# Optimization experiments

Hardware: AMD Instinct MI355X
Metric: run time of the kernel (lower is better)

## Reference

```python
import jax, jax.numpy as jnp
import numpy as np

N = 50000          # nodes
E = 800000         # edges (avg in-degree 16)
NFEAT, F = 128, 64 # input feat, hidden width (outfeat = outd_1 = outd_2 = 64)
ALPHA = 0.2        # leaky relu slope
AVG_LIN = 16.0             # sum(bin*hist)/N for deg histogram (all deg 16)
AVG_LOG = float(np.log(17.0))  # sum(log(bin+1)*hist)/N


def setup_inputs():
    key = jax.random.key(0)
    ks = jax.random.split(key, 16)
    g = lambda i, shp, s: (jax.random.normal(ks[i], shp, jnp.float32) * s)
    return {
        "x": g(0, (N, NFEAT), 1.0),
        "adj": jnp.zeros((1,), jnp.float32),
        "edge_index": jax.random.randint(ks[1], (2, E), 0, N, dtype=jnp.int32),
        "W0": g(2, (NFEAT, F), NFEAT ** -0.5), "b0": jnp.zeros((F,), jnp.float32),
        "c1_pre_W": g(3, (2 * F, F), (2 * F) ** -0.5), "c1_pre_b": jnp.zeros((F,), jnp.float32),
        "c1_post_W": g(4, (5 * F, F), (5 * F) ** -0.5), "c1_post_b": jnp.zeros((F,), jnp.float32),
        "c1_lin_W": g(5, (F, F), F ** -0.5), "c1_lin_b": jnp.zeros((F,), jnp.float32),
        "c2_pre_W": g(6, (2 * F, F), (2 * F) ** -0.5), "c2_pre_b": jnp.zeros((F,), jnp.float32),
        "c2_post_W": g(7, (5 * F, F), (5 * F) ** -0.5), "c2_post_b": jnp.zeros((F,), jnp.float32),
        "c2_lin_W": g(8, (F, F), F ** -0.5), "c2_lin_b": jnp.zeros((F,), jnp.float32),
        "W2": g(9, (F, 1), F ** -0.5), "b2": jnp.zeros((1,), jnp.float32),
    }


def pna_conv(x, src, dst, pre_W, pre_b, post_W, post_b, lin_W, lin_b):
    # message: pre_nn(cat[x_i, x_j]) per edge  (x_i = target, x_j = source)
    h = jnp.concatenate([x[dst], x[src]], axis=-1) @ pre_W + pre_b  # [E, F]
    cnt = jax.ops.segment_sum(jnp.ones((h.shape[0],), h.dtype), dst, num_segments=N)
    deg = jnp.clip(cnt, 1.0)                                        # [N]
    mean = jax.ops.segment_sum(h, dst, num_segments=N) / deg[:, None]
    mx = jax.ops.segment_max(h, dst, num_segments=N)
    mx = jnp.where(cnt[:, None] > 0, mx, 0.0)                       # empty segs -> 0
    agg = jnp.concatenate([mean, mx], axis=-1)                      # [N, 2F]
    att = agg * (AVG_LOG / jnp.log(deg + 1.0))[:, None]             # attenuation scaler
    lin = agg * (deg / AVG_LIN)[:, None]                            # linear scaler
    out = jnp.concatenate([x, att, lin], axis=-1)                   # [N, 5F]
    out = out @ post_W + post_b
    return out @ lin_W + lin_b


def reference(x, adj, edge_index, W0, b0,
              c1_pre_W, c1_pre_b, c1_post_W, c1_post_b, c1_lin_W, c1_lin_b,
              c2_pre_W, c2_pre_b, c2_post_W, c2_post_b, c2_lin_W, c2_lin_b,
              W2, b2):
    src, dst = edge_index[0], edge_index[1]
    h = jax.nn.leaky_relu(x @ W0 + b0, negative_slope=ALPHA)  # dropout = id (eval)
    h = jax.nn.relu(pna_conv(h, src, dst, c1_pre_W, c1_pre_b, c1_post_W, c1_post_b, c1_lin_W, c1_lin_b))
    h = jax.nn.relu(pna_conv(h, src, dst, c2_pre_W, c2_pre_b, c2_post_W, c2_post_b, c2_lin_W, c2_lin_b))
    return h @ W2 + b2  # [N, 1]
```

## Files before the change

kernel.cpp:

```cpp
#include <hip/hip_runtime.h>
#include <hip/hip_bf16.h>

typedef __hip_bfloat16 bf16;
typedef unsigned short u16;
typedef unsigned int u32;
typedef __attribute__((ext_vector_type(8))) short short8;
typedef __attribute__((ext_vector_type(4))) float f32x4;

static constexpr float AVG_LOG_C = 2.8332133440562162f;
#define BCAP 1024
#define CHUNK 4096
#define PREP_TOTAL (8192 * 3 + 20480 * 2 + 64 * 6 + 1)

__device__ __forceinline__ u32 f2bf_bits(float f) {
    u32 u = __float_as_uint(f);
    return (u + 0x7fffu + ((u >> 16) & 1u)) >> 16;
}
__device__ __forceinline__ float bf2f(u16 b) {
    return __uint_as_float(((u32)b) << 16);
}

__global__ __launch_bounds__(1024) void detect_zero_kernel(
    const u32* __restrict__ xwords, int* __restrict__ flag,
    int* __restrict__ bcnt, int nb) {
    if (blockIdx.x == 0) {
        int tid = threadIdx.x;
        if (tid < 64) {
            int good = 0;
            for (int i = tid; i < 2048; i += 64) {
                u32 lo = xwords[i] & 0xffffu;
                float v = __uint_as_float(lo << 16);
                float a = fabsf(v);
                if (v == 0.0f || (a >= 1e-3f && a <= 100.0f)) good++;
            }
            for (int off = 32; off; off >>= 1) good += __shfl_xor(good, off, 64);
            if (tid == 0) *flag = (2 * good > 2048) ? 1 : 0;
        }
    } else {
        int i = (blockIdx.x - 1) * 1024 + threadIdx.x;
        if (i < nb) bcnt[i] = 0;
    }
}

__global__ __launch_bounds__(1024) void prep_scatter_kernel(
    const int* __restrict__ srcs, const int* __restrict__ dsts,
    int* __restrict__ bcnt, u32* __restrict__ bstage, int e, int nb,
    const void* __restrict__ W0r,  const void* __restrict__ b0r,
    const void* __restrict__ pre1r, const void* __restrict__ preb1r,
    const void* __restrict__ post1r, const void* __restrict__ postb1r,
    const void* __restrict__ lin1r, const void* __restrict__ linb1r,
    const void* __restrict__ pre2r, const void* __restrict__ preb2r,
    const void* __restrict__ post2r, const void* __restrict__ postb2r,
    const void* __restrict__ lin2r, const void* __restrict__ linb2r,
    const void* __restrict__ W2r,  const void* __restrict__ b2r,
    u16* __restrict__ W0p, u16* __restrict__ pre1p, u16* __restrict__ pre2p,
    u16* __restrict__ wf1p, u16* __restrict__ wf2p,
    float* __restrict__ bfo1, float* __restrict__ bfo2,
    float* __restrict__ preb1f, float* __restrict__ preb2f,
    float* __restrict__ b0f, float* __restrict__ W2f, float* __restrict__ b2f,
    const int* __restrict__ flag) {
    __shared__ int lhist[2048];
    __shared__ int lbase[2048];
    int tid = threadIdx.x;
    int scatB = (e + CHUNK - 1) / CHUNK;
    if ((int)blockIdx.x < scatB) {
        int cbase = blockIdx.x * CHUNK;
        for (int b = tid; b < nb; b += 1024) lhist[b] = 0;
        __syncthreads();
#pragma unroll
        for (int i = 0; i < CHUNK; i += 1024) {
            int e0 = cbase + i + tid;
            if (e0 < e) atomicAdd(&lhist[dsts[e0] >> 5], 1);
        }
        __syncthreads();
        for (int b = tid; b < nb; b += 1024) {
            int c = lhist[b];
            lbase[b] = c ? atomicAdd(&bcnt[b], c) : 0;
            lhist[b] = 0;
        }
        __syncthreads();
#pragma unroll
        for (int i = 0; i < CHUNK; i += 1024) {
            int e0 = cbase + i + tid;
            if (e0 < e) {
                int d = dsts[e0];
                int b = d >> 5;
                int pos = lbase[b] + atomicAdd(&lhist[b], 1);
                if (pos < BCAP)
                    bstage[(size_t)b * BCAP + pos] = (u32)srcs[e0] | ((u32)(d & 31) << 17);
            }
        }
        return;
    }
    int idx = ((int)blockIdx.x - scatB) * 1024 + tid;
    bool isbf = (*flag) != 0;
    auto ld = [&](const void* p, int i) -> float {
        return isbf ? bf2f(((const u16*)p)[i]) : ((const float*)p)[i];
    };
    if (idx < 8192) {
        int j = idx & 7, l = (idx >> 3) & 63, tt = idx >> 9;
        int c = tt & 3, s = tt >> 2;
        int kk = s * 32 + (l >> 4) * 8 + j;
        int col = c * 16 + (l & 15);
        W0p[idx] = (u16)f2bf_bits(ld(W0r, kk * 64 + col));
        return;
    }
    idx -= 8192;
    for (int which = 0; which < 2; ++which) {
        if (idx < 8192) {
            const void* src = which ? pre2r : pre1r;
            u16* dst = which ? pre2p : pre1p;
            int j = idx & 7, l = (idx >> 3) & 63, tt = idx >> 9;
            int c = tt & 7, s = tt >> 3;
            int kk = s * 32 + (l >> 4) * 8 + j;
            int col = c * 16 + (l & 15);
            float v = (col < 64) ? ld(src, kk * 64 + col)
                                 : ld(src, (64 + kk) * 64 + (col - 64));
            dst[idx] = (u16)f2bf_bits(v);
            return;
        }
        idx -= 8192;
    }
    for (int which = 0; which < 2; ++which) {
        if (idx < 20480) {
            const void* postW = which ? post2r : post1r;
            const void* linW  = which ? lin2r  : lin1r;
            u16* dst = which ? wf2p : wf1p;
            int j = idx & 7, l = (idx >> 3) & 63, tt = idx >> 9;
            int c = tt & 3, s = tt >> 2;
            int kk = s * 32 + (l >> 4) * 8 + j;
            int col = c * 16 + (l & 15);
            float a = 0.f;
            for (int k = 0; k < 64; ++k)
                a = fmaf(ld(postW, kk * 64 + k), ld(linW, k * 64 + col), a);
            dst[idx] = (u16)f2bf_bits(a);
            return;
        }
        idx -= 20480;
    }
    for (int which = 0; which < 2; ++which) {
        if (idx < 64) {
            const void* postb = which ? postb2r : postb1r;
            const void* linW  = which ? lin2r : lin1r;
            const void* linb  = which ? linb2r : linb1r;
            float* dst = which ? bfo2 : bfo1;
            float a = ld(linb, idx);
            for (int k = 0; k < 64; ++k)
                a = fmaf(ld(postb, k), ld(linW, k * 64 + idx), a);
            dst[idx] = a;
            return;
        }
        idx -= 64;
    }
    if (idx < 64) { preb1f[idx] = ld(preb1r, idx); return; }
    idx -= 64;
    if (idx < 64) { preb2f[idx] = ld(preb2r, idx); return; }
    idx -= 64;
    if (idx < 64) { b0f[idx] = ld(b0r, idx); return; }
    idx -= 64;
    if (idx < 64) { W2f[idx] = ld(W2r, idx); return; }
    idx -= 64;
    if (idx < 1) { b2f[0] = ld(b2r, 0); }
}

__global__ __launch_bounds__(512, 6) void gemm_x_pq_kernel(
    const void* __restrict__ xraw, const u16* __restrict__ W0p,
    const float* __restrict__ b0f, const u16* __restrict__ pre1p,
    u16* __restrict__ hA, u16* __restrict__ PQ,
    const int* __restrict__ flag, int n) {
    __shared__ __align__(16) u16 xsh[32 * 136];
    __shared__ __align__(16) u16 hsh[32 * 72];
    int tid = threadIdx.x;
    int wave = __builtin_amdgcn_readfirstlane(tid >> 6);
    int lane = tid & 63;
    int blockbase = blockIdx.x * 32;
    bool isbf = (*flag) != 0;
    {
        int row = tid >> 4;
        int cg = (tid & 15) * 8;
        int grow = blockbase + row;
        short8 v = short8{0, 0, 0, 0, 0, 0, 0, 0};
        if (grow < n) {
            if (isbf) {
                v = *(const short8*)((const u16*)xraw + (size_t)grow * 128 + cg);
            } else {
                const float* xf = (const float*)xraw + (size_t)grow * 128 + cg;
                f32x4 a0 = *(const f32x4*)xf;
                f32x4 a1 = *(const f32x4*)(xf + 4);
#pragma unroll
                for (int j = 0; j < 4; ++j) {
                    v[j]     = (short)f2bf_bits(a0[j]);
                    v[4 + j] = (short)f2bf_bits(a1[j]);
                }
            }
        }
        *(short8*)&xsh[row * 136 + cg] = v;
    }
    __syncthreads();
    int rt = wave & 1, ct = wave >> 1;
    int arl = rt * 16 + (lane & 15);
    int koff = (lane >> 4) * 8;
    f32x4 acc = f32x4{0.f, 0.f, 0.f, 0.f};
#pragma unroll
    for (int s = 0; s < 4; ++s) {
        short8 a = *(const short8*)&xsh[arl * 136 + s * 32 + koff];
        short8 b = *(const short8*)(W0p + ((size_t)(s * 4 + ct) * 64 + lane) * 8);
        acc = __builtin_amdgcn_mfma_f32_16x16x32_bf16(a, b, acc, 0, 0, 0);
    }
    {
        int col = ct * 16 + (lane & 15);
        float bv = b0f[col];
        int r0l = rt * 16 + (lane >> 4) * 4;
#pragma unroll
        for (int r = 0; r < 4; ++r) {
            float v = acc[r] + bv;
            v = v > 0.f ? v : 0.2f * v;
            u16 bits = (u16)f2bf_bits(v);
            hsh[(r0l + r) * 72 + col] = bits;
            int grow = blockbase + r0l + r;
            if (grow < n) hA[(size_t)grow * 64 + col] = bits;
        }
    }
    __syncthreads();
#pragma unroll
    for (int half = 0; half < 2; ++half) {
        int tile = wave * 2 + half;
        int rt2 = tile & 1, ct2 = tile >> 1;
        int ar2 = rt2 * 16 + (lane & 15);
        f32x4 acc2 = f32x4{0.f, 0.f, 0.f, 0.f};
#pragma unroll
        for (int s = 0; s < 2; ++s) {
            short8 a = *(const short8*)&hsh[ar2 * 72 + s * 32 + koff];
            short8 b = *(const short8*)(pre1p + ((size_t)(s * 8 + ct2) * 64 + lane) * 8);
            acc2 = __builtin_amdgcn_mfma_f32_16x16x32_bf16(a, b, acc2, 0, 0, 0);
        }
        int col2 = ct2 * 16 + (lane & 15);
        int r02 = rt2 * 16 + (lane >> 4) * 4;
#pragma unroll
        for (int r = 0; r < 4; ++r) {
            int grow = blockbase + r02 + r;
            if (grow < n) PQ[(size_t)grow * 128 + col2] = (u16)f2bf_bits(acc2[r]);
        }
    }
}

template<int FINAL>
__global__ __launch_bounds__(512, 6) void agg_gemm_kernel(
    const u16* __restrict__ PQ, const u16* __restrict__ h,
    const u32* __restrict__ bstage, const int* __restrict__ bcnt,
    const float* __restrict__ prebf, const u16* __restrict__ Wfp,
    const float* __restrict__ bfo, const u16* __restrict__ prenextp,
    u16* __restrict__ hout, u16* __restrict__ PQout,
    const float* __restrict__ W2f, const float* __restrict__ b2f,
    void* __restrict__ out, const int* __restrict__ flag, int n) {
    constexpr int PAD = 328;
    __shared__ __align__(16) u16 vsh[32 * PAD];
    __shared__ __align__(16) u16 hsh[32 * 72];
    __shared__ u32 lel[BCAP];
    __shared__ int loff[32], lcnt[32], lcur[32];
    __shared__ float fsum[32];
    int tid = threadIdx.x;
    int wave = __builtin_amdgcn_readfirstlane(tid >> 6);
    int lane = tid & 63;
    int b = blockIdx.x;
    int blockbase = b * 32;
    float pbl = prebf[lane];
    if (tid < 32) { lcnt[tid] = 0; if (FINAL) fsum[tid] = 0.f; }
    __syncthreads();
    int cb = min(bcnt[b], BCAP);
    const u32* st = bstage + (size_t)b * BCAP;
    for (int i = tid; i < cb; i += 512) atomicAdd(&lcnt[st[i] >> 17], 1);
    __syncthreads();
    if (wave == 0) {
        int c = (lane < 32) ? lcnt[lane] : 0;
        int s = c;
        for (int off = 1; off < 32; off <<= 1) {
            int t = __shfl_up(s, (unsigned)off, 64);
            if (lane >= off) s += t;
        }
        if (lane < 32) {
            loff[lane] = s - c;
            lcur[lane] = s - c;
        }
    }
    __syncthreads();
    for (int i = tid; i < cb; i += 512) {
        u32 e = st[i];
        int pos = atomicAdd(&lcur[e >> 17], 1);
        lel[pos] = (e & 0x1ffffu) << 8;
    }
    __syncthreads();
    const char* PQc = (const char*)PQ;
    u32 voffb = 128u + 2u * (u32)lane;
#pragma unroll
    for (int t = 0; t < 4; ++t) {
        int nl = wave * 4 + t;
        int node = blockbase + nl;
        u16* vrow = &vsh[nl * PAD];
        if (node < n) {
            int beg = loff[nl], end = beg + lcnt[nl];
            int cnt = end - beg;
            float s = 0.f, m = -3.4e38f;
            int e = beg;
            for (; e + 8 <= end; e += 8) {
                float q0 = bf2f(*(const u16*)(PQc + lel[e]     + voffb));
                float q1 = bf2f(*(const u16*)(PQc + lel[e + 1] + voffb));
                float q2 = bf2f(*(const u16*)(PQc + lel[e + 2] + voffb));
                float q3 = bf2f(*(const u16*)(PQc + lel[e + 3] + voffb));
                float q4 = bf2f(*(const u16*)(PQc + lel[e + 4] + voffb));
                float q5 = bf2f(*(const u16*)(PQc + lel[e + 5] + voffb));
                float q6 = bf2f(*(const u16*)(PQc + lel[e + 6] + voffb));
                float q7 = bf2f(*(const u16*)(PQc + lel[e + 7] + voffb));
                s += ((q0 + q1) + (q2 + q3)) + ((q4 + q5) + (q6 + q7));
                m = fmaxf(m, fmaxf(fmaxf(fmaxf(q0, q1), fmaxf(q2, q3)),
                                   fmaxf(fmaxf(q4, q5), fmaxf(q6, q7))));
            }
            for (; e + 4 <= end; e += 4) {
                float q0 = bf2f(*(const u16*)(PQc + lel[e]     + voffb));
                float q1 = bf2f(*(const u16*)(PQc + lel[e + 1] + voffb));
                float q2 = bf2f(*(const u16*)(PQc + lel[e + 2] + voffb));
                float q3 = bf2f(*(const u16*)(PQc + lel[e + 3] + voffb));
                s += (q0 + q1) + (q2 + q3);
                m = fmaxf(fmaxf(m, fmaxf(q0, q1)), fmaxf(q2, q3));
            }
            for (; e < end; ++e) {
                float q = bf2f(*(const u16*)(PQc + lel[e] + voffb));
                s += q;
                m = fmaxf(m, q);
            }
            float mean, mx, deg;
            if (cnt > 0) {
                deg = (float)cnt;
                float p = bf2f(PQ[(size_t)node * 128 + lane]) + pbl;
                mean = p + s / deg;
                mx = p + m;
            } else {
                deg = 1.f; mean = 0.f; mx = 0.f;
            }
            float att = AVG_LOG_C / logf(deg + 1.f);
            float lin = deg * (1.f / 16.f);
            vrow[lane]       = h[(size_t)node * 64 + lane];
            vrow[64 + lane]  = (u16)f2bf_bits(att * mean);
            vrow[128 + lane] = (u16)f2bf_bits(att * mx);
            vrow[192 + lane] = (u16)f2bf_bits(lin * mean);
            vrow[256 + lane] = (u16)f2bf_bits(lin * mx);
        } else {
            vrow[lane] = 0; vrow[64 + lane] = 0; vrow[128 + lane] = 0;
            vrow[192 + lane] = 0; vrow[256 + lane] = 0;
        }
    }
    __syncthreads();
    int rt = wave & 1, ct = wave >> 1;
    int arl = rt * 16 + (lane & 15);
    int koff = (lane >> 4) * 8;
    f32x4 acc = f32x4{0.f, 0.f, 0.f, 0.f};
#pragma unroll
    for (int s = 0; s < 10; ++s) {
        short8 a = *(const short8*)&vsh[arl * PAD + s * 32 + koff];
        short8 b2 = *(const short8*)(Wfp + ((size_t)(s * 4 + ct) * 64 + lane) * 8);
        acc = __builtin_amdgcn_mfma_f32_16x16x32_bf16(a, b2, acc, 0, 0, 0);
    }
    int col = ct * 16 + (lane & 15);
    float bv = bfo[col];
    int r0l = rt * 16 + (lane >> 4) * 4;
    if constexpr (!FINAL) {
#pragma unroll
        for (int r = 0; r < 4; ++r) {
            float v = fmaxf(acc[r] + bv, 0.f);
            u16 bits = (u16)f2bf_bits(v);
            hsh[(r0l + r) * 72 + col] = bits;
            int grow = blockbase + r0l + r;
            if (grow < n) hout[(size_t)grow * 64 + col] = bits;
        }
        __syncthreads();
#pragma unroll
        for (int half = 0; half < 2; ++half) {
            int tile = wave * 2 + half;
            int rt2 = tile & 1, ct2 = tile >> 1;
            int ar2 = rt2 * 16 + (lane & 15);
            f32x4 acc2 = f32x4{0.f, 0.f, 0.f, 0.f};
#pragma unroll
            for (int s = 0; s < 2; ++s) {
                short8 a = *(const short8*)&hsh[ar2 * 72 + s * 32 + koff];
                short8 b2 = *(const short8*)(prenextp + ((size_t)(s * 8 + ct2) * 64 + lane) * 8);
                acc2 = __builtin_amdgcn_mfma_f32_16x16x32_bf16(a, b2, acc2, 0, 0, 0);
            }
            int col2 = ct2 * 16 + (lane & 15);
            int r02 = rt2 * 16 + (lane >> 4) * 4;
#pragma unroll
            for (int r = 0; r < 4; ++r) {
                int grow = blockbase + r02 + r;
                if (grow < n) PQout[(size_t)grow * 128 + col2] = (u16)f2bf_bits(acc2[r]);
            }
        }
    } else {
        float w2 = W2f[col];
        float part[4];
#pragma unroll
        for (int r = 0; r < 4; ++r)
            part[r] = fmaxf(acc[r] + bv, 0.f) * w2;
#pragma unroll
        for (int r = 0; r < 4; ++r) {
            float v = part[r];
            v += __shfl_xor(v, 1, 64);
            v += __shfl_xor(v, 2, 64);
            v += __shfl_xor(v, 4, 64);
            v += __shfl_xor(v, 8, 64);
            if ((lane & 15) == 0) atomicAdd(&fsum[r0l + r], v);
        }
        __syncthreads();
        if (tid < 32) {
            int grow = blockbase + tid;
            if (grow < n) {
                float res = fsum[tid] + b2f[0];
                if (*flag) ((u16*)out)[grow] = (u16)f2bf_bits(res);
                else       ((float*)out)[grow] = res;
            }
        }
    }
}

extern "C" void kernel_launch(void* const* d_in, const int* in_sizes, int n_in,
                              void* d_out, int out_size, void* d_ws, size_t ws_size,
                              hipStream_t stream) {
    const int N = in_sizes[0] / 128;
    const int E = in_sizes[2] / 2;
    const int nb = (N + 31) >> 5;
    const int* ei = (const int*)d_in[2];
    const int* esrc = ei;
    const int* edst = ei + E;

    char* w = (char*)d_ws;
    auto alloc = [&](size_t bytes) -> void* {
        void* p = (void*)w;
        w += (bytes + 255) & ~(size_t)255;
        return p;
    };
    int* flag    = (int*)alloc(4);
    int* bcnt    = (int*)alloc((size_t)nb * 4);
    u32* bstage  = (u32*)alloc((size_t)nb * BCAP * 4);
    u16* W0p     = (u16*)alloc(128 * 64 * 2);
    u16* pre1p   = (u16*)alloc(64 * 128 * 2);
    u16* pre2p   = (u16*)alloc(64 * 128 * 2);
    u16* wf1p    = (u16*)alloc(320 * 64 * 2);
    u16* wf2p    = (u16*)alloc(320 * 64 * 2);
    float* bfo1  = (float*)alloc(64 * 4);
    float* bfo2  = (float*)alloc(64 * 4);
    float* preb1f= (float*)alloc(64 * 4);
    float* preb2f= (float*)alloc(64 * 4);
    float* b0f   = (float*)alloc(64 * 4);
    float* W2f   = (float*)alloc(64 * 4);
    float* b2f_  = (float*)alloc(4);
    u16* hA      = (u16*)alloc((size_t)N * 64 * 2);
    u16* hB      = (u16*)alloc((size_t)N * 64 * 2);
    u16* PQA     = (u16*)alloc((size_t)N * 128 * 2);
    u16* PQB     = (u16*)alloc((size_t)N * 128 * 2);

    detect_zero_kernel<<<1 + (nb + 1023) / 1024, 1024, 0, stream>>>(
        (const u32*)d_in[0], flag, bcnt, nb);

    int scatB = (E + CHUNK - 1) / CHUNK;
    int prepB = (PREP_TOTAL + 1023) / 1024;
    prep_scatter_kernel<<<scatB + prepB, 1024, 0, stream>>>(
        esrc, edst, bcnt, bstage, E, nb,
        d_in[3], d_in[4], d_in[5], d_in[6], d_in[7], d_in[8], d_in[9], d_in[10],
        d_in[11], d_in[12], d_in[13], d_in[14], d_in[15], d_in[16], d_in[17], d_in[18],
        W0p, pre1p, pre2p, wf1p, wf2p,
        bfo1, bfo2, preb1f, preb2f, b0f, W2f, b2f_, flag);

    int gblocks = (N + 31) / 32;
    gemm_x_pq_kernel<<<gblocks, 512, 0, stream>>>(
        d_in[0], W0p, b0f, pre1p, hA, PQA, flag, N);

    agg_gemm_kernel<0><<<gblocks, 512, 0, stream>>>(
        PQA, hA, bstage, bcnt, preb1f, wf1p, bfo1, pre2p, hB, PQB,
        nullptr, nullptr, nullptr, flag, N);

    agg_gemm_kernel<1><<<gblocks, 512, 0, stream>>>(
        PQB, hB, bstage, bcnt, preb2f, wf2p, bfo2, nullptr, nullptr, nullptr,
        W2f, b2f_, d_out, flag, N);
}
```

Baseline: 204.6 us.

## Fuse scatter, first GEMM and both PNA aggregations into cooperative persistent kernel

```diff
diff --git a/kernel.cpp b/kernel.cpp
--- a/kernel.cpp
+++ b/kernel.cpp
@@ -1,5 +1,8 @@
 #include <hip/hip_runtime.h>
 #include <hip/hip_bf16.h>
+#include <hip/hip_cooperative_groups.h>
+
+namespace cg = cooperative_groups;
 
 typedef __hip_bfloat16 bf16;
 typedef unsigned short u16;
@@ -9,7 +12,7 @@
 
 static constexpr float AVG_LOG_C = 2.8332133440562162f;
 #define BCAP 1024
-#define CHUNK 4096
+#define CHUNK 2048
 #define PREP_TOTAL (8192 * 3 + 20480 * 2 + 64 * 6 + 1)
 
 __device__ __forceinline__ u32 f2bf_bits(float f) {
@@ -20,31 +23,31 @@
     return __uint_as_float(((u32)b) << 16);
 }
 
-__global__ __launch_bounds__(1024) void detect_zero_kernel(
+struct KParams {
+    const void* xraw;
+    const int* srcs;
+    const int* dsts;
+    int* bcnt;
+    u32* bstage;
+    const u16 *W0p, *pre1p, *pre2p, *wf1p, *wf2p;
+    const float *b0f, *preb1f, *preb2f, *bfo1, *bfo2, *W2f, *b2f;
+    u16 *hA, *hB, *PQA, *PQB;
+    void* out;
+    const int* flag;
+    int n, e, nb, scatChunks, gB;
+};
+
+struct SMem {
+    union {
+        struct { int lhist[2048]; int lbase[2048]; } sc;
+        struct { __align__(16) u16 xsh[32 * 136]; __align__(16) u16 hsh[32 * 72]; } gx;
+        struct { __align__(16) u16 vsh[32 * 328]; __align__(16) u16 hsh[32 * 72];
+                 u32 lel[BCAP]; int loff[32]; int lcnt[32]; int lcur[32]; float fsum[32]; } ag;
+    };
+};
+
+__global__ __launch_bounds__(1024) void prep_weights_kernel(
     const u32* __restrict__ xwords, int* __restrict__ flag,
-    int* __restrict__ bcnt, int nb) {
-    if (blockIdx.x == 0) {
-        int tid = threadIdx.x;
-        if (tid < 64) {
-            int good = 0;
-            for (int i = tid; i < 2048; i += 64) {
-                u32 lo = xwords[i] & 0xffffu;
-                float v = __uint_as_float(lo << 16);
-                float a = fabsf(v);
-                if (v == 0.0f || (a >= 1e-3f && a <= 100.0f)) good++;
-            }
-            for (int off = 32; off; off >>= 1) good += __shfl_xor(good, off, 64);
-            if (tid == 0) *flag = (2 * good > 2048) ? 1 : 0;
-        }
-    } else {
-        int i = (blockIdx.x - 1) * 1024 + threadIdx.x;
-        if (i < nb) bcnt[i] = 0;
-    }
-}
-
-__global__ __launch_bounds__(1024) void prep_scatter_kernel(
-    const int* __restrict__ srcs, const int* __restrict__ dsts,
-    int* __restrict__ bcnt, u32* __restrict__ bstage, int e, int nb,
     const void* __restrict__ W0r,  const void* __restrict__ b0r,
     const void* __restrict__ pre1r, const void* __restrict__ preb1r,
     const void* __restrict__ post1r, const void* __restrict__ postb1r,
@@ -57,46 +60,27 @@
     u16* __restrict__ wf1p, u16* __restrict__ wf2p,
     float* __restrict__ bfo1, float* __restrict__ bfo2,
     float* __restrict__ preb1f, float* __restrict__ preb2f,
-    float* __restrict__ b0f, float* __restrict__ W2f, float* __restrict__ b2f,
-    const int* __restrict__ flag) {
-    __shared__ int lhist[2048];
-    __shared__ int lbase[2048];
+    float* __restrict__ b0f, float* __restrict__ W2f, float* __restrict__ b2f) {
+    __shared__ int sflag;
     int tid = threadIdx.x;
-    int scatB = (e + CHUNK - 1) / CHUNK;
-    if ((int)blockIdx.x < scatB) {
-        int cbase = blockIdx.x * CHUNK;
-        for (int b = tid; b < nb; b += 1024) lhist[b] = 0;
-        __syncthreads();
-#pragma unroll
-        for (int i = 0; i < CHUNK; i += 1024) {
-            int e0 = cbase + i + tid;
-            if (e0 < e) atomicAdd(&lhist[dsts[e0] >> 5], 1);
-        }
-        __syncthreads();
-        for (int b = tid; b < nb; b += 1024) {
-            int c = lhist[b];
-            lbase[b] = c ? atomicAdd(&bcnt[b], c) : 0;
-            lhist[b] = 0;
-        }
-        __syncthreads();
-#pragma unroll
-        for (int i = 0; i < CHUNK; i += 1024) {
-            int e0 = cbase + i + tid;
-            if (e0 < e) {
-                int d = dsts[e0];
-                int b = d >> 5;
-                int pos = lbase[b] + atomicAdd(&lhist[b], 1);
-                if (pos < BCAP)
-                    bstage[(size_t)b * BCAP + pos] = (u32)srcs[e0] | ((u32)(d & 31) << 17);
-            }
-        }
-        return;
-    }
-    int idx = ((int)blockIdx.x - scatB) * 1024 + tid;
-    bool isbf = (*flag) != 0;
+    if (tid < 64) {
+        int good = 0;
+        for (int i = tid; i < 2048; i += 64) {
+            u32 lo = xwords[i] & 0xffffu;
+            float v = __uint_as_float(lo << 16);
+            float a = fabsf(v);
+            if (v == 0.0f || (a >= 1e-3f && a <= 100.0f)) good++;
+        }
+        for (int off = 32; off; off >>= 1) good += __shfl_xor(good, off, 64);
+        if (tid == 0) sflag = (2 * good > 2048) ? 1 : 0;
+    }
+    __syncthreads();
+    bool isbf = sflag != 0;
+    if (blockIdx.x == 0 && tid == 0) *flag = sflag;
     auto ld = [&](const void* p, int i) -> float {
         return isbf ? bf2f(((const u16*)p)[i]) : ((const float*)p)[i];
     };
+    int idx = (int)blockIdx.x * 1024 + tid;
     if (idx < 8192) {
         int j = idx & 7, l = (idx >> 3) & 63, tt = idx >> 9;
         int c = tt & 3, s = tt >> 2;
@@ -163,28 +147,48 @@
     if (idx < 1) { b2f[0] = ld(b2r, 0); }
 }
 
-__global__ __launch_bounds__(512, 6) void gemm_x_pq_kernel(
-    const void* __restrict__ xraw, const u16* __restrict__ W0p,
-    const float* __restrict__ b0f, const u16* __restrict__ pre1p,
-    u16* __restrict__ hA, u16* __restrict__ PQ,
-    const int* __restrict__ flag, int n) {
-    __shared__ __align__(16) u16 xsh[32 * 136];
-    __shared__ __align__(16) u16 hsh[32 * 72];
-    int tid = threadIdx.x;
-    int wave = __builtin_amdgcn_readfirstlane(tid >> 6);
-    int lane = tid & 63;
-    int blockbase = blockIdx.x * 32;
-    bool isbf = (*flag) != 0;
+__device__ __forceinline__ void scatter_chunk(SMem& sm, const KParams& p, int chunk, int tid) {
+    for (int bb = tid; bb < p.nb; bb += 512) sm.sc.lhist[bb] = 0;
+    __syncthreads();
+    int cbase = chunk * CHUNK;
+#pragma unroll
+    for (int i = 0; i < CHUNK; i += 512) {
+        int e0 = cbase + i + tid;
+        if (e0 < p.e) atomicAdd(&sm.sc.lhist[p.dsts[e0] >> 5], 1);
+    }
+    __syncthreads();
+    for (int bb = tid; bb < p.nb; bb += 512) {
+        int c = sm.sc.lhist[bb];
+        sm.sc.lbase[bb] = c ? atomicAdd(&p.bcnt[bb], c) : 0;
+        sm.sc.lhist[bb] = 0;
+    }
+    __syncthreads();
+#pragma unroll
+    for (int i = 0; i < CHUNK; i += 512) {
+        int e0 = cbase + i + tid;
+        if (e0 < p.e) {
+            int d = p.dsts[e0];
+            int bb = d >> 5;
+            int pos = sm.sc.lbase[bb] + atomicAdd(&sm.sc.lhist[bb], 1);
+            if (pos < BCAP)
+                p.bstage[(size_t)bb * BCAP + pos] = (u32)p.srcs[e0] | ((u32)(d & 31) << 17);
+        }
+    }
+}
+
+__device__ __forceinline__ void gemm_bucket(SMem& sm, const KParams& p, int g,
+                                            bool isbf, int wave, int lane, int tid) {
+    int blockbase = g * 32;
     {
         int row = tid >> 4;
-        int cg = (tid & 15) * 8;
+        int cgx = (tid & 15) * 8;
         int grow = blockbase + row;
         short8 v = short8{0, 0, 0, 0, 0, 0, 0, 0};
-        if (grow < n) {
+        if (grow < p.n) {
             if (isbf) {
-                v = *(const short8*)((const u16*)xraw + (size_t)grow * 128 + cg);
+                v = *(const short8*)((const u16*)p.xraw + (size_t)grow * 128 + cgx);
             } else {
-                const float* xf = (const float*)xraw + (size_t)grow * 128 + cg;
+                const float* xf = (const float*)p.xraw + (size_t)grow * 128 + cgx;
                 f32x4 a0 = *(const f32x4*)xf;
                 f32x4 a1 = *(const f32x4*)(xf + 4);
 #pragma unroll
@@ -194,7 +198,7 @@
                 }
             }
         }
-        *(short8*)&xsh[row * 136 + cg] = v;
+        *(short8*)&sm.gx.xsh[row * 136 + cgx] = v;
     }
     __syncthreads();
     int rt = wave & 1, ct = wave >> 1;
@@ -203,22 +207,22 @@
     f32x4 acc = f32x4{0.f, 0.f, 0.f, 0.f};
 #pragma unroll
     for (int s = 0; s < 4; ++s) {
-        short8 a = *(const short8*)&xsh[arl * 136 + s * 32 + koff];
-        short8 b = *(const short8*)(W0p + ((size_t)(s * 4 + ct) * 64 + lane) * 8);
+        short8 a = *(const short8*)&sm.gx.xsh[arl * 136 + s * 32 + koff];
+        short8 b = *(const short8*)(p.W0p + ((size_t)(s * 4 + ct) * 64 + lane) * 8);
         acc = __builtin_amdgcn_mfma_f32_16x16x32_bf16(a, b, acc, 0, 0, 0);
     }
     {
         int col = ct * 16 + (lane & 15);
-        float bv = b0f[col];
+        float bv = p.b0f[col];
         int r0l = rt * 16 + (lane >> 4) * 4;
 #pragma unroll
         for (int r = 0; r < 4; ++r) {
             float v = acc[r] + bv;
             v = v > 0.f ? v : 0.2f * v;
             u16 bits = (u16)f2bf_bits(v);
-            hsh[(r0l + r) * 72 + col] = bits;
+            sm.gx.hsh[(r0l + r) * 72 + col] = bits;
             int grow = blockbase + r0l + r;
-            if (grow < n) hA[(size_t)grow * 64 + col] = bits;
+            if (grow < p.n) p.hA[(size_t)grow * 64 + col] = bits;
         }
     }
     __syncthreads();
@@ -230,8 +234,8 @@
         f32x4 acc2 = f32x4{0.f, 0.f, 0.f, 0.f};
 #pragma unroll
         for (int s = 0; s < 2; ++s) {
-            short8 a = *(const short8*)&hsh[ar2 * 72 + s * 32 + koff];
-            short8 b = *(const short8*)(pre1p + ((size_t)(s * 8 + ct2) * 64 + lane) * 8);
+            short8 a = *(const short8*)&sm.gx.hsh[ar2 * 72 + s * 32 + koff];
+            short8 b = *(const short8*)(p.pre1p + ((size_t)(s * 8 + ct2) * 64 + lane) * 8);
             acc2 = __builtin_amdgcn_mfma_f32_16x16x32_bf16(a, b, acc2, 0, 0, 0);
         }
         int col2 = ct2 * 16 + (lane & 15);
@@ -239,55 +243,40 @@
 #pragma unroll
         for (int r = 0; r < 4; ++r) {
             int grow = blockbase + r02 + r;
-            if (grow < n) PQ[(size_t)grow * 128 + col2] = (u16)f2bf_bits(acc2[r]);
+            if (grow < p.n) p.PQA[(size_t)grow * 128 + col2] = (u16)f2bf_bits(acc2[r]);
         }
     }
 }
 
 template<int FINAL>
-__global__ __launch_bounds__(512, 6) void agg_gemm_kernel(
+__device__ __forceinline__ void agg_bucket(
+    SMem& sm, const KParams& p, int b, bool isbf, int wave, int lane, int tid,
     const u16* __restrict__ PQ, const u16* __restrict__ h,
-    const u32* __restrict__ bstage, const int* __restrict__ bcnt,
     const float* __restrict__ prebf, const u16* __restrict__ Wfp,
     const float* __restrict__ bfo, const u16* __restrict__ prenextp,
-    u16* __restrict__ hout, u16* __restrict__ PQout,
-    const float* __restrict__ W2f, const float* __restrict__ b2f,
-    void* __restrict__ out, const int* __restrict__ flag, int n) {
-    constexpr int PAD = 328;
-    __shared__ __align__(16) u16 vsh[32 * PAD];
-    __shared__ __align__(16) u16 hsh[32 * 72];
-    __shared__ u32 lel[BCAP];
-    __shared__ int loff[32], lcnt[32], lcur[32];
-    __shared__ float fsum[32];
-    int tid = threadIdx.x;
-    int wave = __builtin_amdgcn_readfirstlane(tid >> 6);
-    int lane = tid & 63;
-    int b = blockIdx.x;
+    u16* __restrict__ hout, u16* __restrict__ PQout) {
     int blockbase = b * 32;
     float pbl = prebf[lane];
-    if (tid < 32) { lcnt[tid] = 0; if (FINAL) fsum[tid] = 0.f; }
-    __syncthreads();
-    int cb = min(bcnt[b], BCAP);
-    const u32* st = bstage + (size_t)b * BCAP;
-    for (int i = tid; i < cb; i += 512) atomicAdd(&lcnt[st[i] >> 17], 1);
+    if (tid < 32) { sm.ag.lcnt[tid] = 0; if (FINAL) sm.ag.fsum[tid] = 0.f; }
+    __syncthreads();
+    int cb = min(p.bcnt[b], BCAP);
+    const u32* st = p.bstage + (size_t)b * BCAP;
+    for (int i = tid; i < cb; i += 512) atomicAdd(&sm.ag.lcnt[st[i] >> 17], 1);
     __syncthreads();
     if (wave == 0) {
-        int c = (lane < 32) ? lcnt[lane] : 0;
+        int c = (lane < 32) ? sm.ag.lcnt[lane] : 0;
         int s = c;
         for (int off = 1; off < 32; off <<= 1) {
             int t = __shfl_up(s, (unsigned)off, 64);
             if (lane >= off) s += t;
         }
-        if (lane < 32) {
-            loff[lane] = s - c;
-            lcur[lane] = s - c;
-        }
+        if (lane < 32) { sm.ag.loff[lane] = s - c; sm.ag.lcur[lane] = s - c; }
     }
     __syncthreads();
     for (int i = tid; i < cb; i += 512) {
-        u32 e = st[i];
-        int pos = atomicAdd(&lcur[e >> 17], 1);
-        lel[pos] = (e & 0x1ffffu) << 8;
+        u32 ev = st[i];
+        int pos = atomicAdd(&sm.ag.lcur[ev >> 17], 1);
+        sm.ag.lel[pos] = (ev & 0x1ffffu) << 8;
     }
     __syncthreads();
     const char* PQc = (const char*)PQ;
@@ -296,44 +285,44 @@
     for (int t = 0; t < 4; ++t) {
         int nl = wave * 4 + t;
         int node = blockbase + nl;
-        u16* vrow = &vsh[nl * PAD];
-        if (node < n) {
-            int beg = loff[nl], end = beg + lcnt[nl];
+        u16* vrow = &sm.ag.vsh[nl * 328];
+        if (node < p.n) {
+            int beg = sm.ag.loff[nl], end = beg + sm.ag.lcnt[nl];
             int cnt = end - beg;
             float s = 0.f, m = -3.4e38f;
-            int e = beg;
-            for (; e + 8 <= end; e += 8) {
-                float q0 = bf2f(*(const u16*)(PQc + lel[e]     + voffb));
-                float q1 = bf2f(*(const u16*)(PQc + lel[e + 1] + voffb));
-                float q2 = bf2f(*(const u16*)(PQc + lel[e + 2] + voffb));
-                float q3 = bf2f(*(const u16*)(PQc + lel[e + 3] + voffb));
-                float q4 = bf2f(*(const u16*)(PQc + lel[e + 4] + voffb));
-                float q5 = bf2f(*(const u16*)(PQc + lel[e + 5] + voffb));
-                float q6 = bf2f(*(const u16*)(PQc + lel[e + 6] + voffb));
-                float q7 = bf2f(*(const u16*)(PQc + lel[e + 7] + voffb));
+            int ei = beg;
+            for (; ei + 8 <= end; ei += 8) {
+                float q0 = bf2f(*(const u16*)(PQc + sm.ag.lel[ei]     + voffb));
+                float q1 = bf2f(*(const u16*)(PQc + sm.ag.lel[ei + 1] + voffb));
+                float q2 = bf2f(*(const u16*)(PQc + sm.ag.lel[ei + 2] + voffb));
+                float q3 = bf2f(*(const u16*)(PQc + sm.ag.lel[ei + 3] + voffb));
+                float q4 = bf2f(*(const u16*)(PQc + sm.ag.lel[ei + 4] + voffb));
+                float q5 = bf2f(*(const u16*)(PQc + sm.ag.lel[ei + 5] + voffb));
+                float q6 = bf2f(*(const u16*)(PQc + sm.ag.lel[ei + 6] + voffb));
+                float q7 = bf2f(*(const u16*)(PQc + sm.ag.lel[ei + 7] + voffb));
                 s += ((q0 + q1) + (q2 + q3)) + ((q4 + q5) + (q6 + q7));
                 m = fmaxf(m, fmaxf(fmaxf(fmaxf(q0, q1), fmaxf(q2, q3)),
                                    fmaxf(fmaxf(q4, q5), fmaxf(q6, q7))));
             }
-            for (; e + 4 <= end; e += 4) {
-                float q0 = bf2f(*(const u16*)(PQc + lel[e]     + voffb));
-                float q1 = bf2f(*(const u16*)(PQc + lel[e + 1] + voffb));
-                float q2 = bf2f(*(const u16*)(PQc + lel[e + 2] + voffb));
-                float q3 = bf2f(*(const u16*)(PQc + lel[e + 3] + voffb));
+            for (; ei + 4 <= end; ei += 4) {
+                float q0 = bf2f(*(const u16*)(PQc + sm.ag.lel[ei]     + voffb));
+                float q1 = bf2f(*(const u16*)(PQc + sm.ag.lel[ei + 1] + voffb));
+                float q2 = bf2f(*(const u16*)(PQc + sm.ag.lel[ei + 2] + voffb));
+                float q3 = bf2f(*(const u16*)(PQc + sm.ag.lel[ei + 3] + voffb));
                 s += (q0 + q1) + (q2 + q3);
                 m = fmaxf(fmaxf(m, fmaxf(q0, q1)), fmaxf(q2, q3));
             }
-            for (; e < end; ++e) {
-                float q = bf2f(*(const u16*)(PQc + lel[e] + voffb));
+            for (; ei < end; ++ei) {
+                float q = bf2f(*(const u16*)(PQc + sm.ag.lel[ei] + voffb));
                 s += q;
                 m = fmaxf(m, q);
             }
             float mean, mx, deg;
             if (cnt > 0) {
                 deg = (float)cnt;
-                float p = bf2f(PQ[(size_t)node * 128 + lane]) + pbl;
-                mean = p + s / deg;
-                mx = p + m;
+                float pv = bf2f(PQ[(size_t)node * 128 + lane]) + pbl;
+                mean = pv + s / deg;
+                mx = pv + m;
             } else {
                 deg = 1.f; mean = 0.f; mx = 0.f;
             }
@@ -356,7 +345,7 @@
     f32x4 acc = f32x4{0.f, 0.f, 0.f, 0.f};
 #pragma unroll
     for (int s = 0; s < 10; ++s) {
-        short8 a = *(const short8*)&vsh[arl * PAD + s * 32 + koff];
+        short8 a = *(const short8*)&sm.ag.vsh[arl * 328 + s * 32 + koff];
         short8 b2 = *(const short8*)(Wfp + ((size_t)(s * 4 + ct) * 64 + lane) * 8);
         acc = __builtin_amdgcn_mfma_f32_16x16x32_bf16(a, b2, acc, 0, 0, 0);
     }
@@ -368,9 +357,9 @@
         for (int r = 0; r < 4; ++r) {
             float v = fmaxf(acc[r] + bv, 0.f);
             u16 bits = (u16)f2bf_bits(v);
-            hsh[(r0l + r) * 72 + col] = bits;
+            sm.ag.hsh[(r0l + r) * 72 + col] = bits;
             int grow = blockbase + r0l + r;
-            if (grow < n) hout[(size_t)grow * 64 + col] = bits;
+            if (grow < p.n) hout[(size_t)grow * 64 + col] = bits;
         }
         __syncthreads();
 #pragma unroll
@@ -381,7 +370,7 @@
             f32x4 acc2 = f32x4{0.f, 0.f, 0.f, 0.f};
 #pragma unroll
             for (int s = 0; s < 2; ++s) {
-                short8 a = *(const short8*)&hsh[ar2 * 72 + s * 32 + koff];
+                short8 a = *(const short8*)&sm.ag.hsh[ar2 * 72 + s * 32 + koff];
                 short8 b2 = *(const short8*)(prenextp + ((size_t)(s * 8 + ct2) * 64 + lane) * 8);
                 acc2 = __builtin_amdgcn_mfma_f32_16x16x32_bf16(a, b2, acc2, 0, 0, 0);
             }
@@ -390,11 +379,11 @@
 #pragma unroll
             for (int r = 0; r < 4; ++r) {
                 int grow = blockbase + r02 + r;
-                if (grow < n) PQout[(size_t)grow * 128 + col2] = (u16)f2bf_bits(acc2[r]);
+                if (grow < p.n) PQout[(size_t)grow * 128 + col2] = (u16)f2bf_bits(acc2[r]);
             }
         }
     } else {
-        float w2 = W2f[col];
+        float w2 = p.W2f[col];
         float part[4];
 #pragma unroll
         for (int r = 0; r < 4; ++r)
@@ -406,18 +395,86 @@
             v += __shfl_xor(v, 2, 64);
             v += __shfl_xor(v, 4, 64);
             v += __shfl_xor(v, 8, 64);
-            if ((lane & 15) == 0) atomicAdd(&fsum[r0l + r], v);
+            if ((lane & 15) == 0) atomicAdd(&sm.ag.fsum[r0l + r], v);
         }
         __syncthreads();
         if (tid < 32) {
             int grow = blockbase + tid;
-            if (grow < n) {
-                float res = fsum[tid] + b2f[0];
-                if (*flag) ((u16*)out)[grow] = (u16)f2bf_bits(res);
-                else       ((float*)out)[grow] = res;
-            }
-        }
-    }
+            if (grow < p.n) {
+                float res = sm.ag.fsum[tid] + p.b2f[0];
+                if (isbf) ((u16*)p.out)[grow] = (u16)f2bf_bits(res);
+                else      ((float*)p.out)[grow] = res;
+            }
+        }
+        __syncthreads();
+    }
+}
+
+__device__ __forceinline__ void phaseA_body(SMem& sm, const KParams& p, bool isbf,
+                                            int wave, int lane, int tid, int gstride) {
+    int nA = p.scatChunks + p.gB;
+    for (int w = blockIdx.x; w < nA; w += gstride) {
+        if (w < p.scatChunks) scatter_chunk(sm, p, w, tid);
+        else gemm_bucket(sm, p, w - p.scatChunks, isbf, wave, lane, tid);
+        __syncthreads();
+    }
+}
+__device__ __forceinline__ void phaseB_body(SMem& sm, const KParams& p, bool isbf,
+                                            int wave, int lane, int tid, int gstride) {
+    for (int b = blockIdx.x; b < p.gB; b += gstride) {
+        agg_bucket<0>(sm, p, b, isbf, wave, lane, tid,
+                      p.PQA, p.hA, p.preb1f, p.wf1p, p.bfo1, p.pre2p, p.hB, p.PQB);
+        __syncthreads();
+    }
+}
+__device__ __forceinline__ void phaseC_body(SMem& sm, const KParams& p, bool isbf,
+                                            int wave, int lane, int tid, int gstride) {
+    for (int b = blockIdx.x; b < p.gB; b += gstride) {
+        agg_bucket<1>(sm, p, b, isbf, wave, lane, tid,
+                      p.PQB, p.hB, p.preb2f, p.wf2p, p.bfo2, nullptr, nullptr, nullptr);
+        __syncthreads();
+    }
+}
+
+__global__ __launch_bounds__(512, 4) void fused_kernel(KParams p) {
+    __shared__ SMem sm;
+    cg::grid_group grid = cg::this_grid();
+    int tid = threadIdx.x;
+    int wave = __builtin_amdgcn_readfirstlane(tid >> 6);
+    int lane = tid & 63;
+    bool isbf = (*p.flag) != 0;
+    phaseA_body(sm, p, isbf, wave, lane, tid, (int)gridDim.x);
+    __threadfence();
+    grid.sync();
+    phaseB_body(sm, p, isbf, wave, lane, tid, (int)gridDim.x);
+    __threadfence();
+    grid.sync();
+    phaseC_body(sm, p, isbf, wave, lane, tid, (int)gridDim.x);
+}
+
+__global__ __launch_bounds__(512, 4) void phaseA_kernel(KParams p) {
+    __shared__ SMem sm;
+    int tid = threadIdx.x;
+    int wave = __builtin_amdgcn_readfirstlane(tid >> 6);
+    int lane = tid & 63;
+    bool isbf = (*p.flag) != 0;
+    phaseA_body(sm, p, isbf, wave, lane, tid, (int)gridDim.x);
+}
+__global__ __launch_bounds__(512, 4) void phaseB_kernel(KParams p) {
+    __shared__ SMem sm;
+    int tid = threadIdx.x;
+    int wave = __builtin_amdgcn_readfirstlane(tid >> 6);
+    int lane = tid & 63;
+    bool isbf = (*p.flag) != 0;
+    phaseB_body(sm, p, isbf, wave, lane, tid, (int)gridDim.x);
+}
+__global__ __launch_bounds__(512, 4) void phaseC_kernel(KParams p) {
+    __shared__ SMem sm;
+    int tid = threadIdx.x;
+    int wave = __builtin_amdgcn_readfirstlane(tid >> 6);
+    int lane = tid & 63;
+    bool isbf = (*p.flag) != 0;
+    phaseC_body(sm, p, isbf, wave, lane, tid, (int)gridDim.x);
 }
 
 extern "C" void kernel_launch(void* const* d_in, const int* in_sizes, int n_in,
@@ -456,27 +513,58 @@
     u16* PQA     = (u16*)alloc((size_t)N * 128 * 2);
     u16* PQB     = (u16*)alloc((size_t)N * 128 * 2);
 
-    detect_zero_kernel<<<1 + (nb + 1023) / 1024, 1024, 0, stream>>>(
-        (const u32*)d_in[0], flag, bcnt, nb);
-
-    int scatB = (E + CHUNK - 1) / CHUNK;
+    hipMemsetAsync(bcnt, 0, (size_t)nb * 4, stream);
+
     int prepB = (PREP_TOTAL + 1023) / 1024;
-    prep_scatter_kernel<<<scatB + prepB, 1024, 0, stream>>>(
-        esrc, edst, bcnt, bstage, E, nb,
+    prep_weights_kernel<<<prepB, 1024, 0, stream>>>(
+        (const u32*)d_in[0], flag,
         d_in[3], d_in[4], d_in[5], d_in[6], d_in[7], d_in[8], d_in[9], d_in[10],
         d_in[11], d_in[12], d_in[13], d_in[14], d_in[15], d_in[16], d_in[17], d_in[18],
         W0p, pre1p, pre2p, wf1p, wf2p,
-        bfo1, bfo2, preb1f, preb2f, b0f, W2f, b2f_, flag);
-
-    int gblocks = (N + 31) / 32;
-    gemm_x_pq_kernel<<<gblocks, 512, 0, stream>>>(
-        d_in[0], W0p, b0f, pre1p, hA, PQA, flag, N);
-
-    agg_gemm_kernel<0><<<gblocks, 512, 0, stream>>>(
-        PQA, hA, bstage, bcnt, preb1f, wf1p, bfo1, pre2p, hB, PQB,
-        nullptr, nullptr, nullptr, flag, N);
-
-    agg_gemm_kernel<1><<<gblocks, 512, 0, stream>>>(
-        PQB, hB, bstage, bcnt, preb2f, wf2p, bfo2, nullptr, nullptr, nullptr,
-        W2f, b2f_, d_out, flag, N);
-}
+        bfo1, bfo2, preb1f, preb2f, b0f, W2f, b2f_);
+
+    KParams hp;
+    hp.xraw = d_in[0]; hp.srcs = esrc; hp.dsts = edst;
+    hp.bcnt = bcnt; hp.bstage = bstage;
+    hp.W0p = W0p; hp.pre1p = pre1p; hp.pre2p = pre2p; hp.wf1p = wf1p; hp.wf2p = wf2p;
+    hp.b0f = b0f; hp.preb1f = preb1f; hp.preb2f = preb2f;
+    hp.bfo1 = bfo1; hp.bfo2 = bfo2; hp.W2f = W2f; hp.b2f = b2f_;
+    hp.hA = hA; hp.hB = hB; hp.PQA = PQA; hp.PQB = PQB;
+    hp.out = d_out; hp.flag = flag;
+    hp.n = N; hp.e = E; hp.nb = nb;
+    hp.scatChunks = (E + CHUNK - 1) / CHUNK;
+    hp.gB = (N + 31) / 32;
+
+    static int coopGrid = -1;
+    if (coopGrid < 0) {
+        int maxB = 0;
+        hipError_t oe = hipOccupancyMaxActiveBlocksPerMultiprocessor(
+            &maxB, reinterpret_cast<const void*>(&fused_kernel), 512, 0);
+        int cus = 0, dev = 0;
+        hipGetDevice(&dev);
+        hipDeviceGetAttribute(&cus, hipDeviceAttributeMultiprocessorCount, dev);
+        if (oe == hipSuccess && maxB > 0 && cus > 0) {
+            long g = (long)maxB * cus;
+            if (g > 1024) g = 1024;
+            coopGrid = (int)g;
+        } else {
+            coopGrid = 0;
+        }
+    }
+
+    bool coopOK = false;
+    if (coopGrid > 0) {
+        void* args[] = { (void*)&hp };
+        hipError_t ce = hipLaunchCooperativeKernel(
+            reinterpret_cast<const void*>(&fused_kernel),
+            dim3((unsigned)coopGrid), dim3(512), args, 0, stream);
+        coopOK = (ce == hipSuccess);
+        if (!coopOK) coopGrid = 0;
+    }
+    if (!coopOK) {
+        int nA = hp.scatChunks + hp.gB;
+        phaseA_kernel<<<nA, 512, 0, stream>>>(hp);
+        phaseB_kernel<<<hp.gB, 512, 0, stream>>>(hp);
+        phaseC_kernel<<<hp.gB, 512, 0, stream>>>(hp);
+    }
+}
```

Result: slower. 507.7 us (+148.1%).
